# Performance work log

Hardware: AMD Instinct MI355X
Metric: run time of the kernel (lower is better)

Reference implementation:

```python
import jax, jax.numpy as jnp
import numpy as np
import string

N_QUBITS = 16
N_LAYERS = 2
BATCH = 32
DIM = 2 ** N_QUBITS


def _apply_1q(psi, U, q):
    # psi: (B,) + (2,)*n complex; U: (2,2) complex acting on qubit q
    n = psi.ndim - 1
    ax = string.ascii_lowercase[:n]
    out = list(ax)
    out[q] = 'A'
    return jnp.einsum('A' + ax[q] + ',z' + ax + '->z' + ''.join(out), U, psi)


def _apply_2q(psi, G, c, t):
    # G: (2,2,2,2) = (out_c, out_t, in_c, in_t)
    n = psi.ndim - 1
    ax = string.ascii_lowercase[:n]
    out = list(ax)
    out[c] = 'A'
    out[t] = 'B'
    return jnp.einsum('AB' + ax[c] + ax[t] + ',z' + ax + '->z' + ''.join(out), G, psi)


def _rx(th):
    c = jnp.cos(th * 0.5).astype(jnp.complex64)
    s = jnp.sin(th * 0.5).astype(jnp.complex64)
    return jnp.array([[c, -1j * s], [-1j * s, c]])


def _ry(th):
    c = jnp.cos(th * 0.5).astype(jnp.complex64)
    s = jnp.sin(th * 0.5).astype(jnp.complex64)
    return jnp.array([[c, -s], [s, c]])


def _rz(th):
    th_c = th.astype(jnp.complex64)
    z = jnp.zeros((), jnp.complex64)
    return jnp.array([[jnp.exp(-0.5j * th_c), z], [z, jnp.exp(0.5j * th_c)]])


_CNOT = jnp.array([[1, 0, 0, 0],
                   [0, 1, 0, 0],
                   [0, 0, 0, 1],
                   [0, 0, 1, 0]], dtype=jnp.complex64).reshape(2, 2, 2, 2)


def setup_inputs() -> dict:
    key = jax.random.key(0)
    k1, k2, k3 = jax.random.split(key, 3)
    thetas = jax.random.normal(k1, (N_LAYERS, 3, N_QUBITS), dtype=jnp.float32)
    re = jax.random.normal(k2, (BATCH, DIM), dtype=jnp.float32)
    im = jax.random.normal(k3, (BATCH, DIM), dtype=jnp.float32)
    norm = jnp.sqrt(jnp.sum(re * re + im * im, axis=-1, keepdims=True))
    return {"thetas": thetas, "state_re": re / norm, "state_im": im / norm}


def reference(thetas, state_re, state_im):
    B = state_re.shape[0]
    psi = (state_re.astype(jnp.complex64) + 1j * state_im.astype(jnp.complex64))
    psi = psi.reshape((B,) + (2,) * N_QUBITS)
    for l in range(N_LAYERS):
        for q in range(N_QUBITS):
            psi = _apply_1q(psi, _rx(thetas[l, 0, q]), q)
            psi = _apply_1q(psi, _ry(thetas[l, 1, q]), q)
            psi = _apply_1q(psi, _rz(thetas[l, 2, q]), q)
        for q in range(N_QUBITS):
            psi = _apply_2q(psi, _CNOT, q, (q + 1) % N_QUBITS)
    probs = (psi.real ** 2 + psi.imag ** 2).reshape(B, -1)
    return probs
```

## Files before the change

### kernel.cpp

```cpp
#include <hip/hip_runtime.h>
#include <hip/hip_fp16.h>


#define NT 256

__device__ __forceinline__ int fperm(int x) {
  int y = x ^ (x >> 1);
  y ^= (x & 1) ? 0xC000 : 0;
  return y & 0xFFFF;
}

__device__ __forceinline__ int finv16(int x) {
  int s = x;
  s ^= s >> 1; s ^= s >> 2; s ^= s >> 4; s ^= s >> 8;
  int b15 = ((s ^ (s >> 15)) & 1) << 15;
  return (s & 0x7FFF) | b15;
}

__device__ __forceinline__ int swz(int l) { return l ^ ((l >> 4) & 15); }

__device__ __forceinline__ __half2 packa(float2 a) {
  return __floats2half2_rn(a.x, a.y);
}
__device__ __forceinline__ float2 unpacka(__half2 h) {
  return __half22float2(h);
}

__device__ __forceinline__ void compute_gates(const float* __restrict__ th, float* gsh) {
  int tid = threadIdx.x;
  if (tid < 32) {
    int l = tid >> 4, q = tid & 15;
    float tx = th[l * 48 + q], ty = th[l * 48 + 16 + q], tz = th[l * 48 + 32 + q];
    float cx, sx, cy, sy, cz, sz;
    sincosf(0.5f * tx, &sx, &cx);
    sincosf(0.5f * ty, &sy, &cy);
    sincosf(0.5f * tz, &sz, &cz);
    float m00r = cy * cx, m00i =  sy * sx;
    float m01r = -sy * cx, m01i = -cy * sx;
    float m10r =  sy * cx, m10i = -cy * sx;
    float m11r =  cy * cx, m11i = -sy * sx;
    float* G = gsh + tid * 8;
    G[0] = cz * m00r + sz * m00i;  G[1] = cz * m00i - sz * m00r;
    G[2] = cz * m01r + sz * m01i;  G[3] = cz * m01i - sz * m01r;
    G[4] = cz * m10r - sz * m10i;  G[5] = cz * m10i + sz * m10r;
    G[6] = cz * m11r - sz * m11i;  G[7] = cz * m11i + sz * m11r;
  }
}

template <int MK, int SK, int N>
__device__ __forceinline__ void greg(float2 (&a)[N], const float* G, int c) {
  const float4* G4 = (const float4*)G;
  float4 r0 = G4[0], r1 = G4[1];
  bool sw = (c != 0);
  float h00r = sw ? r1.z : r0.x, h00i = sw ? r1.w : r0.y;
  float h01r = sw ? r1.x : r0.z, h01i = sw ? r1.y : r0.w;
  float h10r = sw ? r0.z : r1.x, h10i = sw ? r0.w : r1.y;
  float h11r = sw ? r0.x : r1.z, h11i = sw ? r0.y : r1.w;
  constexpr int PV = MK & (-MK);
#pragma unroll
  for (int k = 0; k < N; k++) {
    if (k & PV) continue;
    const int k2 = k ^ MK;
    const int p0 = __builtin_popcount(k & SK) & 1;
    const int ka = p0 ? k2 : k;
    const int kb = p0 ? k : k2;
    float2 x = a[ka], y = a[kb];
    a[ka] = make_float2(h00r * x.x - h00i * x.y + h01r * y.x - h01i * y.y,
                        h00r * x.y + h00i * x.x + h01r * y.y + h01i * y.x);
    a[kb] = make_float2(h10r * x.x - h10i * x.y + h11r * y.x - h11i * y.y,
                        h10r * x.y + h10i * x.x + h11r * y.y + h11i * y.x);
  }
}


__global__ void __launch_bounds__(NT, 2) pass1_k(const float* __restrict__ th,
                                                 const float* __restrict__ xre,
                                                 const float* __restrict__ xim,
                                                 __half2* __restrict__ ws) {
  __shared__ float gsh[256];
  __shared__ float2 samp[4096];
  int t = threadIdx.x, blk = blockIdx.x;
  int batch = (blk & 7) + ((blk >> 7) << 3), wb = (blk >> 3) & 15;
  int bbase = batch << 16;
  float2 a[16];
  int base = bbase + (wb << 12);
  const float4* xr4 = (const float4*)(xre + base + (t << 4));
  const float4* xi4 = (const float4*)(xim + base + (t << 4));
#pragma unroll
  for (int q = 0; q < 4; q++) {
    float4 v = xr4[q], w = xi4[q];
    a[4*q+0] = make_float2(v.x, w.x); a[4*q+1] = make_float2(v.y, w.y);
    a[4*q+2] = make_float2(v.z, w.z); a[4*q+3] = make_float2(v.w, w.w);
  }
  compute_gates(th, gsh);
  __syncthreads();
  greg<1, 1>(a, gsh + 15 * 8, 0);
  greg<2, 2>(a, gsh + 14 * 8, 0);
  greg<4, 4>(a, gsh + 13 * 8, 0);
  greg<8, 8>(a, gsh + 12 * 8, 0);
#pragma unroll
  for (int k = 0; k < 16; k++) samp[swz((t << 4) | k)] = a[k];
  __syncthreads();
#pragma unroll
  for (int k = 0; k < 16; k++)
    a[k] = samp[swz((t & 15) | (k << 4) | ((t >> 4) << 8))];
  greg<1, 1>(a, gsh + 11 * 8, 0);
  greg<2, 2>(a, gsh + 10 * 8, 0);
  greg<4, 4>(a, gsh + 9 * 8, 0);
  greg<8, 8>(a, gsh + 8 * 8, 0);
#pragma unroll
  for (int k = 0; k < 16; k++)
    samp[swz((t & 15) | (k << 4) | ((t >> 4) << 8))] = a[k];
  __syncthreads();
#pragma unroll
  for (int k = 0; k < 16; k++) a[k] = samp[swz(t | (k << 8))];
  greg<1, 1>(a, gsh + 7 * 8, 0);
  greg<2, 2>(a, gsh + 6 * 8, 0);
  greg<4, 4>(a, gsh + 5 * 8, 0);
  greg<8, 8>(a, gsh + 4 * 8, 0);
#pragma unroll
  for (int k = 0; k < 16; k++)
    ws[base + t + (k << 8)] = packa(a[k]);
}


__global__ void __launch_bounds__(NT, 2) pass2_k(const float* __restrict__ th,
                                                 __half2* __restrict__ ws) {
  __shared__ float gsh[256];
  __shared__ float2 samp[4096];
  int t = threadIdx.x, blk = blockIdx.x;
  int batch = (blk & 7) + ((blk >> 7) << 3), wb = (blk >> 3) & 15;
  int bbase = batch << 16;
  float2 a[16];
#pragma unroll
  for (int k = 0; k < 16; k++)
    a[k] = unpacka(ws[bbase + t + (wb << 8) + (k << 12)]);
  compute_gates(th, gsh);
  __syncthreads();
  int cA = (__popc(t) + __popc(wb)) & 1;
  greg<1, 1>(a, gsh + 3 * 8, 0);
  greg<2, 2>(a, gsh + 2 * 8, 0);
  greg<4, 4>(a, gsh + 1 * 8, 0);
  greg<8, 8>(a, gsh + 0 * 8, 0);
  greg<12, 7>(a, gsh + (16 + 0) * 8, cA);
  greg<6, 12>(a, gsh + (16 + 1) * 8, 0);
  greg<3, 14>(a, gsh + (16 + 2) * 8, 0);
#pragma unroll
  for (int k = 0; k < 16; k++) samp[swz(t | (k << 8))] = a[k];
  __syncthreads();
#pragma unroll
  for (int k = 0; k < 16; k++)
    a[k] = samp[swz((k & 3) | (t << 2) | ((k >> 2) << 10))];
  greg<13, 15>(a, gsh + (16 + 15) * 8, cA);
  greg<3, 14>(a, gsh + (16 + 14) * 8, cA);
#pragma unroll
  for (int k = 0; k < 16; k++)
    samp[swz((k & 3) | (t << 2) | ((k >> 2) << 10))] = a[k];
  __syncthreads();
#pragma unroll
  for (int k = 0; k < 16; k++)
    a[k] = samp[swz((t & 1) | (k << 1) | ((t >> 1) << 5))];
  {
    int cC = (__popc(t >> 1) + __popc(wb)) & 1;
    greg<3, 14>(a, gsh + (16 + 13) * 8, cC);
    greg<6, 12>(a, gsh + (16 + 12) * 8, cC);
    greg<12, 8>(a, gsh + (16 + 11) * 8, cC);
  }
#pragma unroll
  for (int k = 0; k < 16; k++)
    samp[swz((t & 1) | (k << 1) | ((t >> 1) << 5))] = a[k];
  __syncthreads();
#pragma unroll
  for (int k = 0; k < 16; k++)
    a[k] = samp[swz((t & 15) | (k << 4) | ((t >> 4) << 8))];
  {
    int cD = (__popc(t >> 4) + __popc(wb)) & 1;
    greg<3, 14>(a, gsh + (16 + 10) * 8, cD);
    greg<6, 12>(a, gsh + (16 + 9) * 8, cD);
    greg<12, 8>(a, gsh + (16 + 8) * 8, cD);
  }
#pragma unroll
  for (int k = 0; k < 16; k++) {
    int full = (t & 15) | (k << 4) | (wb << 8) | ((t >> 4) << 12);
    ws[bbase + full] = packa(a[k]);
  }
}


__global__ void __launch_bounds__(NT, 2) pass3_k(const float* __restrict__ th,
                                                 const __half2* __restrict__ ws,
                                                 float* __restrict__ out) {
  __shared__ float gsh[256];
  __shared__ float2 samp[4096];
  int t = threadIdx.x, blk = blockIdx.x;
  int batch = (blk & 7) + ((blk >> 7) << 3), wb = (blk >> 3) & 15;
  int bbase = batch << 16;
  int fix = ((wb & 1) << 7) | ((wb >> 1) << 13);
  int jt = (t & 127) | ((t >> 7) << 8) | fix;
  float2 a[16];
#pragma unroll
  for (int k = 0; k < 16; k++) {
    int j = jt | (k << 9);
    a[k] = unpacka(ws[bbase + fperm(j)]);
  }
  compute_gates(th, gsh);
  __syncthreads();
  greg<1, 1>(a, gsh + (16 + 6) * 8, 0);
  greg<2, 2>(a, gsh + (16 + 5) * 8, 0);
  greg<4, 4>(a, gsh + (16 + 4) * 8, 0);
  greg<8, 8>(a, gsh + (16 + 3) * 8, 0);
#pragma unroll
  for (int k = 0; k < 16; k++) samp[swz(t | (k << 8))] = a[k];
  __syncthreads();
#pragma unroll
  for (int k = 0; k < 16; k++)
    a[k] = samp[swz((t & 127) | (k << 7) | ((t >> 7) << 11))];
  greg<1, 1>(a, gsh + (16 + 7) * 8, 0);
#pragma unroll
  for (int k = 0; k < 16; k++) {
    int l = (t & 127) | (k << 7) | ((t >> 7) << 11);
    int j = (l & 127) | (((l >> 7) & 1) << 8) | ((l >> 8) << 9) | fix;
    float pr = a[k].x * a[k].x + a[k].y * a[k].y;
    __builtin_nontemporal_store(pr, &out[bbase + finv16(j)]);
  }
}


extern "C" void kernel_launch(void* const* d_in, const int* in_sizes, int n_in,
                              void* d_out, int out_size, void* d_ws, size_t ws_size,
                              hipStream_t stream) {
  const float* th  = (const float*)d_in[0];
  const float* xre = (const float*)d_in[1];
  const float* xim = (const float*)d_in[2];
  float* out = (float*)d_out;

  __half2* amp = (__half2*)d_ws;

  pass1_k<<<512, NT, 0, stream>>>(th, xre, xim, amp);
  pass2_k<<<512, NT, 0, stream>>>(th, amp);
  pass3_k<<<512, NT, 0, stream>>>(th, amp, out);
}
```

Before: 104.5 us.

## Use 512-thread blocks with 8 amplitudes per thread across all passes

Doubles threads per block to 512 and halves per-thread register amplitudes from 16 to 8, so each shared-memory exchange stage applies at most three qubit gates instead of four. Pass 2 and pass 3 get new gate schedules and shuffle layouts, and the LDS swizzle is extended with higher address bits to limit bank conflicts. The aim is more waves in flight and less register pressure to hide latency, at the cost of more __syncthreads and LDS round trips, especially in pass 2.

```diff
diff --git a/kernel.cpp b/kernel.cpp
--- a/kernel.cpp
+++ b/kernel.cpp
@@ -2,7 +2,7 @@
 #include <hip/hip_fp16.h>
 
 
-#define NT 256
+#define NT 512
 
 __device__ __forceinline__ int fperm(int x) {
   int y = x ^ (x >> 1);
@@ -17,14 +17,12 @@
   return (s & 0x7FFF) | b15;
 }
 
-__device__ __forceinline__ int swz(int l) { return l ^ ((l >> 4) & 15); }
-
-__device__ __forceinline__ __half2 packa(float2 a) {
-  return __floats2half2_rn(a.x, a.y);
-}
-__device__ __forceinline__ float2 unpacka(__half2 h) {
-  return __half22float2(h);
-}
+__device__ __forceinline__ int swz(int l) {
+  return l ^ (((l >> 4) ^ (l >> 7)) & 15);
+}
+
+__device__ __forceinline__ __half2 packa(float2 a) { return __floats2half2_rn(a.x, a.y); }
+__device__ __forceinline__ float2 unpacka(__half2 h) { return __half22float2(h); }
 
 __device__ __forceinline__ void compute_gates(const float* __restrict__ th, float* gsh) {
   int tid = threadIdx.x;
@@ -47,8 +45,8 @@
   }
 }
 
-template <int MK, int SK, int N>
-__device__ __forceinline__ void greg(float2 (&a)[N], const float* G, int c) {
+template <int MK, int SK>
+__device__ __forceinline__ void greg(float2 (&a)[8], const float* G, int c) {
   const float4* G4 = (const float4*)G;
   float4 r0 = G4[0], r1 = G4[1];
   bool sw = (c != 0);
@@ -58,7 +56,7 @@
   float h11r = sw ? r0.x : r1.z, h11i = sw ? r0.y : r1.w;
   constexpr int PV = MK & (-MK);
 #pragma unroll
-  for (int k = 0; k < N; k++) {
+  for (int k = 0; k < 8; k++) {
     if (k & PV) continue;
     const int k2 = k ^ MK;
     const int p0 = __builtin_popcount(k & SK) & 1;
@@ -73,7 +71,7 @@
 }
 
 
-__global__ void __launch_bounds__(NT, 2) pass1_k(const float* __restrict__ th,
+__global__ void __launch_bounds__(NT, 4) pass1_k(const float* __restrict__ th,
                                                  const float* __restrict__ xre,
                                                  const float* __restrict__ xim,
                                                  __half2* __restrict__ ws) {
@@ -81,113 +79,154 @@
   __shared__ float2 samp[4096];
   int t = threadIdx.x, blk = blockIdx.x;
   int batch = (blk & 7) + ((blk >> 7) << 3), wb = (blk >> 3) & 15;
-  int bbase = batch << 16;
-  float2 a[16];
-  int base = bbase + (wb << 12);
-  const float4* xr4 = (const float4*)(xre + base + (t << 4));
-  const float4* xi4 = (const float4*)(xim + base + (t << 4));
-#pragma unroll
-  for (int q = 0; q < 4; q++) {
-    float4 v = xr4[q], w = xi4[q];
-    a[4*q+0] = make_float2(v.x, w.x); a[4*q+1] = make_float2(v.y, w.y);
-    a[4*q+2] = make_float2(v.z, w.z); a[4*q+3] = make_float2(v.w, w.w);
+  int base = (batch << 16) + (wb << 12);
+  float2 a[8];
+  {
+    const float4* xr4 = (const float4*)(xre + base + (t << 3));
+    const float4* xi4 = (const float4*)(xim + base + (t << 3));
+#pragma unroll
+    for (int q = 0; q < 2; q++) {
+      float4 v = xr4[q], w = xi4[q];
+      a[4*q+0] = make_float2(v.x, w.x); a[4*q+1] = make_float2(v.y, w.y);
+      a[4*q+2] = make_float2(v.z, w.z); a[4*q+3] = make_float2(v.w, w.w);
+    }
   }
   compute_gates(th, gsh);
   __syncthreads();
   greg<1, 1>(a, gsh + 15 * 8, 0);
   greg<2, 2>(a, gsh + 14 * 8, 0);
   greg<4, 4>(a, gsh + 13 * 8, 0);
-  greg<8, 8>(a, gsh + 12 * 8, 0);
-#pragma unroll
-  for (int k = 0; k < 16; k++) samp[swz((t << 4) | k)] = a[k];
-  __syncthreads();
-#pragma unroll
-  for (int k = 0; k < 16; k++)
-    a[k] = samp[swz((t & 15) | (k << 4) | ((t >> 4) << 8))];
-  greg<1, 1>(a, gsh + 11 * 8, 0);
-  greg<2, 2>(a, gsh + 10 * 8, 0);
-  greg<4, 4>(a, gsh + 9 * 8, 0);
-  greg<8, 8>(a, gsh + 8 * 8, 0);
-#pragma unroll
-  for (int k = 0; k < 16; k++)
-    samp[swz((t & 15) | (k << 4) | ((t >> 4) << 8))] = a[k];
-  __syncthreads();
-#pragma unroll
-  for (int k = 0; k < 16; k++) a[k] = samp[swz(t | (k << 8))];
-  greg<1, 1>(a, gsh + 7 * 8, 0);
-  greg<2, 2>(a, gsh + 6 * 8, 0);
-  greg<4, 4>(a, gsh + 5 * 8, 0);
-  greg<8, 8>(a, gsh + 4 * 8, 0);
-#pragma unroll
-  for (int k = 0; k < 16; k++)
-    ws[base + t + (k << 8)] = packa(a[k]);
-}
-
-
-__global__ void __launch_bounds__(NT, 2) pass2_k(const float* __restrict__ th,
+#pragma unroll
+  for (int k = 0; k < 8; k++) samp[swz((t << 3) | k)] = a[k];
+  __syncthreads();
+#pragma unroll
+  for (int k = 0; k < 8; k++)
+    a[k] = samp[swz((t & 7) | (k << 3) | ((t >> 3) << 6))];
+  greg<1, 1>(a, gsh + 12 * 8, 0);
+  greg<2, 2>(a, gsh + 11 * 8, 0);
+  greg<4, 4>(a, gsh + 10 * 8, 0);
+#pragma unroll
+  for (int k = 0; k < 8; k++)
+    samp[swz((t & 7) | (k << 3) | ((t >> 3) << 6))] = a[k];
+  __syncthreads();
+#pragma unroll
+  for (int k = 0; k < 8; k++)
+    a[k] = samp[swz((t & 63) | (k << 6) | ((t >> 6) << 9))];
+  greg<1, 1>(a, gsh + 9 * 8, 0);
+  greg<2, 2>(a, gsh + 8 * 8, 0);
+  greg<4, 4>(a, gsh + 7 * 8, 0);
+#pragma unroll
+  for (int k = 0; k < 8; k++)
+    samp[swz((t & 63) | (k << 6) | ((t >> 6) << 9))] = a[k];
+  __syncthreads();
+#pragma unroll
+  for (int k = 0; k < 8; k++) a[k] = samp[swz(t | (k << 9))];
+  greg<1, 1>(a, gsh + 6 * 8, 0);
+  greg<2, 2>(a, gsh + 5 * 8, 0);
+  greg<4, 4>(a, gsh + 4 * 8, 0);
+#pragma unroll
+  for (int k = 0; k < 8; k++)
+    ws[base + t + (k << 9)] = packa(a[k]);
+}
+
+
+__global__ void __launch_bounds__(NT, 4) pass2_k(const float* __restrict__ th,
                                                  __half2* __restrict__ ws) {
   __shared__ float gsh[256];
   __shared__ float2 samp[4096];
   int t = threadIdx.x, blk = blockIdx.x;
   int batch = (blk & 7) + ((blk >> 7) << 3), wb = (blk >> 3) & 15;
   int bbase = batch << 16;
-  float2 a[16];
-#pragma unroll
-  for (int k = 0; k < 16; k++)
-    a[k] = unpacka(ws[bbase + t + (wb << 8) + (k << 12)]);
+  float2 a[8];
+#pragma unroll
+  for (int k = 0; k < 8; k++) {
+    int g = (t & 255) | (wb << 8) | (((t >> 8) & 1) << 12) | (k << 13);
+    a[k] = unpacka(ws[bbase + g]);
+  }
   compute_gates(th, gsh);
   __syncthreads();
-  int cA = (__popc(t) + __popc(wb)) & 1;
-  greg<1, 1>(a, gsh + 3 * 8, 0);
-  greg<2, 2>(a, gsh + 2 * 8, 0);
-  greg<4, 4>(a, gsh + 1 * 8, 0);
-  greg<8, 8>(a, gsh + 0 * 8, 0);
-  greg<12, 7>(a, gsh + (16 + 0) * 8, cA);
-  greg<6, 12>(a, gsh + (16 + 1) * 8, 0);
-  greg<3, 14>(a, gsh + (16 + 2) * 8, 0);
-#pragma unroll
-  for (int k = 0; k < 16; k++) samp[swz(t | (k << 8))] = a[k];
-  __syncthreads();
-#pragma unroll
-  for (int k = 0; k < 16; k++)
-    a[k] = samp[swz((k & 3) | (t << 2) | ((k >> 2) << 10))];
-  greg<13, 15>(a, gsh + (16 + 15) * 8, cA);
-  greg<3, 14>(a, gsh + (16 + 14) * 8, cA);
-#pragma unroll
-  for (int k = 0; k < 16; k++)
-    samp[swz((k & 3) | (t << 2) | ((k >> 2) << 10))] = a[k];
-  __syncthreads();
-#pragma unroll
-  for (int k = 0; k < 16; k++)
-    a[k] = samp[swz((t & 1) | (k << 1) | ((t >> 1) << 5))];
-  {
-    int cC = (__popc(t >> 1) + __popc(wb)) & 1;
-    greg<3, 14>(a, gsh + (16 + 13) * 8, cC);
-    greg<6, 12>(a, gsh + (16 + 12) * 8, cC);
-    greg<12, 8>(a, gsh + (16 + 11) * 8, cC);
-  }
-#pragma unroll
-  for (int k = 0; k < 16; k++)
-    samp[swz((t & 1) | (k << 1) | ((t >> 1) << 5))] = a[k];
-  __syncthreads();
-#pragma unroll
-  for (int k = 0; k < 16; k++)
-    a[k] = samp[swz((t & 15) | (k << 4) | ((t >> 4) << 8))];
-  {
-    int cD = (__popc(t >> 4) + __popc(wb)) & 1;
-    greg<3, 14>(a, gsh + (16 + 10) * 8, cD);
-    greg<6, 12>(a, gsh + (16 + 9) * 8, cD);
-    greg<12, 8>(a, gsh + (16 + 8) * 8, cD);
-  }
-#pragma unroll
-  for (int k = 0; k < 16; k++) {
-    int full = (t & 15) | (k << 4) | (wb << 8) | ((t >> 4) << 12);
-    ws[bbase + full] = packa(a[k]);
-  }
-}
-
-
-__global__ void __launch_bounds__(NT, 2) pass3_k(const float* __restrict__ th,
+  greg<1, 1>(a, gsh + 2 * 8, 0);
+  greg<2, 2>(a, gsh + 1 * 8, 0);
+  greg<4, 4>(a, gsh + 0 * 8, 0);
+  greg<3, 6>(a, gsh + (16 + 1) * 8, 0);
+#pragma unroll
+  for (int k = 0; k < 8; k++) samp[swz(t | (k << 9))] = a[k];
+  __syncthreads();
+#pragma unroll
+  for (int k = 0; k < 8; k++)
+    a[k] = samp[swz((k & 1) | ((t & 127) << 1) | (((k >> 1) & 3) << 8) | ((t >> 7) << 10))];
+  {
+    int cB = __popc(t >> 7) & 1;
+    greg<2, 2>(a, gsh + 3 * 8, 0);
+    greg<6, 4>(a, gsh + (16 + 2) * 8, cB);
+  }
+#pragma unroll
+  for (int k = 0; k < 8; k++)
+    samp[swz((k & 1) | ((t & 127) << 1) | (((k >> 1) & 3) << 8) | ((t >> 7) << 10))] = a[k];
+  __syncthreads();
+#pragma unroll
+  for (int k = 0; k < 8; k++)
+    a[k] = samp[swz((k & 1) | (t << 1) | ((k >> 1) << 10))];
+  {
+    int cC = (__popc(t) + __popc(wb)) & 1;
+    greg<6, 3>(a, gsh + (16 + 0) * 8, cC);
+    greg<7, 7>(a, gsh + (16 + 15) * 8, cC);
+  }
+#pragma unroll
+  for (int k = 0; k < 8; k++)
+    samp[swz((k & 1) | (t << 1) | ((k >> 1) << 10))] = a[k];
+  __syncthreads();
+#pragma unroll
+  for (int k = 0; k < 8; k++) a[k] = samp[swz(k | (t << 3))];
+  {
+    int cD = (__popc(t) + __popc(wb)) & 1;
+    greg<3, 6>(a, gsh + (16 + 14) * 8, cD);
+    greg<6, 4>(a, gsh + (16 + 13) * 8, cD);
+  }
+#pragma unroll
+  for (int k = 0; k < 8; k++) samp[swz(k | (t << 3))] = a[k];
+  __syncthreads();
+#pragma unroll
+  for (int k = 0; k < 8; k++)
+    a[k] = samp[swz((t & 3) | (k << 2) | ((t >> 2) << 5))];
+  {
+    int cE = (__popc(t >> 2) + __popc(wb)) & 1;
+    greg<3, 6>(a, gsh + (16 + 12) * 8, cE);
+    greg<6, 4>(a, gsh + (16 + 11) * 8, cE);
+  }
+#pragma unroll
+  for (int k = 0; k < 8; k++)
+    samp[swz((t & 3) | (k << 2) | ((t >> 2) << 5))] = a[k];
+  __syncthreads();
+#pragma unroll
+  for (int k = 0; k < 8; k++)
+    a[k] = samp[swz((t & 15) | (k << 4) | ((t >> 4) << 7))];
+  {
+    int cF = (__popc(t >> 4) + __popc(wb)) & 1;
+    greg<3, 6>(a, gsh + (16 + 10) * 8, cF);
+    greg<6, 4>(a, gsh + (16 + 9) * 8, cF);
+  }
+#pragma unroll
+  for (int k = 0; k < 8; k++)
+    samp[swz((t & 15) | (k << 4) | ((t >> 4) << 7))] = a[k];
+  __syncthreads();
+#pragma unroll
+  for (int k = 0; k < 8; k++)
+    a[k] = samp[swz((t & 63) | (k << 6) | ((t >> 6) << 9))];
+  {
+    int cG = (__popc(t >> 6) + __popc(wb)) & 1;
+    greg<3, 6>(a, gsh + (16 + 8) * 8, cG);
+  }
+#pragma unroll
+  for (int k = 0; k < 8; k++) {
+    int l = (t & 63) | (k << 6) | ((t >> 6) << 9);
+    int g = (l & 255) | (wb << 8) | ((l >> 8) << 12);
+    ws[bbase + g] = packa(a[k]);
+  }
+}
+
+
+__global__ void __launch_bounds__(NT, 4) pass3_k(const float* __restrict__ th,
                                                  const __half2* __restrict__ ws,
                                                  float* __restrict__ out) {
   __shared__ float gsh[256];
@@ -196,29 +235,30 @@
   int batch = (blk & 7) + ((blk >> 7) << 3), wb = (blk >> 3) & 15;
   int bbase = batch << 16;
   int fix = ((wb & 1) << 7) | ((wb >> 1) << 13);
-  int jt = (t & 127) | ((t >> 7) << 8) | fix;
-  float2 a[16];
-#pragma unroll
-  for (int k = 0; k < 16; k++) {
-    int j = jt | (k << 9);
+  float2 a[8];
+#pragma unroll
+  for (int k = 0; k < 8; k++) {
+    int l = (t & 127) | (k << 7) | ((t >> 7) << 10);
+    int j = (l & 127) | (((l >> 7) & 1) << 8) | ((l >> 8) << 9) | fix;
     a[k] = unpacka(ws[bbase + fperm(j)]);
   }
   compute_gates(th, gsh);
   __syncthreads();
-  greg<1, 1>(a, gsh + (16 + 6) * 8, 0);
-  greg<2, 2>(a, gsh + (16 + 5) * 8, 0);
-  greg<4, 4>(a, gsh + (16 + 4) * 8, 0);
-  greg<8, 8>(a, gsh + (16 + 3) * 8, 0);
-#pragma unroll
-  for (int k = 0; k < 16; k++) samp[swz(t | (k << 8))] = a[k];
-  __syncthreads();
-#pragma unroll
-  for (int k = 0; k < 16; k++)
-    a[k] = samp[swz((t & 127) | (k << 7) | ((t >> 7) << 11))];
   greg<1, 1>(a, gsh + (16 + 7) * 8, 0);
-#pragma unroll
-  for (int k = 0; k < 16; k++) {
-    int l = (t & 127) | (k << 7) | ((t >> 7) << 11);
+  greg<2, 2>(a, gsh + (16 + 6) * 8, 0);
+  greg<4, 4>(a, gsh + (16 + 5) * 8, 0);
+#pragma unroll
+  for (int k = 0; k < 8; k++)
+    samp[swz((t & 127) | (k << 7) | ((t >> 7) << 10))] = a[k];
+  __syncthreads();
+#pragma unroll
+  for (int k = 0; k < 8; k++)
+    a[k] = samp[swz((k & 1) | (t << 1) | ((k >> 1) << 10))];
+  greg<2, 2>(a, gsh + (16 + 4) * 8, 0);
+  greg<4, 4>(a, gsh + (16 + 3) * 8, 0);
+#pragma unroll
+  for (int k = 0; k < 8; k++) {
+    int l = (k & 1) | (t << 1) | ((k >> 1) << 10);
     int j = (l & 127) | (((l >> 7) & 1) << 8) | ((l >> 8) << 9) | fix;
     float pr = a[k].x * a[k].x + a[k].y * a[k].y;
     __builtin_nontemporal_store(pr, &out[bbase + finv16(j)]);
```

Result: no change. 104.9 us (+0.3%).
